# Kernel tuning notes

Measured on AMD Instinct MI355X. Metric: run time of the kernel, lower is better.

## Reference

```python
import jax, jax.numpy as jnp
import numpy as np
import math

N_HEADS = 16
ROPE_THETA = 10000.0


def setup_inputs() -> dict:
    key = jax.random.key(0)
    ks = jax.random.split(key, 5)
    B, S, D = 2, 2048, 2048
    scale = 1.0 / math.sqrt(D)
    hidden_states = jax.random.normal(ks[0], (B, S, D), dtype=jnp.float32)
    attention_mask = jnp.ones((B, S), dtype=jnp.float32)
    Wq = jax.random.normal(ks[1], (D, D), dtype=jnp.float32) * scale
    Wk = jax.random.normal(ks[2], (D, D), dtype=jnp.float32) * scale
    Wv = jax.random.normal(ks[3], (D, D), dtype=jnp.float32) * scale
    Wo = jax.random.normal(ks[4], (D, D), dtype=jnp.float32) * scale
    return {"hidden_states": hidden_states, "attention_mask": attention_mask,
            "Wq": Wq, "Wk": Wk, "Wv": Wv, "Wo": Wo}


def _rope(x, head_dim):
    # x: [B, H, S, hd]
    S = x.shape[2]
    inv_freq = 1.0 / (ROPE_THETA ** (jnp.arange(0, head_dim, 2, dtype=jnp.float32) / head_dim))
    t = jnp.arange(S, dtype=jnp.float32)
    freqs = t[:, None] * inv_freq[None, :]              # [S, hd/2]
    emb = jnp.concatenate([freqs, freqs], axis=-1)      # [S, hd]
    cos = jnp.cos(emb)[None, None, :, :]
    sin = jnp.sin(emb)[None, None, :, :]
    half = head_dim // 2
    x_rot = jnp.concatenate([-x[..., half:], x[..., :half]], axis=-1)
    return x * cos + x_rot * sin


def reference(hidden_states, attention_mask, Wq, Wk, Wv, Wo):
    B, S, D = hidden_states.shape
    H = N_HEADS
    hd = D // H
    # projections (torch Linear: y = x @ W.T), split heads -> [B, H, S, hd]
    q = (hidden_states @ Wq.T).reshape(B, S, H, hd).transpose(0, 2, 1, 3)
    k = (hidden_states @ Wk.T).reshape(B, S, H, hd).transpose(0, 2, 1, 3)
    v = (hidden_states @ Wv.T).reshape(B, S, H, hd).transpose(0, 2, 1, 3)
    q = _rope(q, hd)
    k = _rope(k, hd)
    scores = jnp.einsum('bhqd,bhkd->bhqk', q, k) / jnp.sqrt(jnp.float32(hd))
    causal = jnp.triu(jnp.ones((S, S), dtype=bool), 1)
    scores = jnp.where(causal[None, None, :, :], -jnp.inf, scores)
    # faithful to the source: mask==0 -> -inf, else the mask value is ADDED
    am = attention_mask[:, None, None, :]
    am = jnp.where(am == 0, -jnp.inf, am)
    scores = scores + am
    attn = jax.nn.softmax(scores.astype(jnp.float32), axis=-1).astype(scores.dtype)
    out = jnp.einsum('bhqk,bhkd->bhqd', attn, v)
    out = out.transpose(0, 2, 1, 3).reshape(B, S, D)
    return out @ Wo.T
```

## Files before the change

kernel.cpp:

```cpp
#include <hip/hip_runtime.h>
#include <hip/hip_bf16.h>

typedef unsigned short u16;
using short8 = __attribute__((ext_vector_type(8))) short;
using s16x4  = __attribute__((ext_vector_type(4))) short;
using f32x4  = __attribute__((ext_vector_type(4))) float;

#define S_LEN   2048
#define D_MODEL 2048
#define N_HEADS 16
#define HEAD_DIM 128

__device__ __forceinline__ float bf2f(u16 u) {
  union { unsigned int i; float f; } c; c.i = ((unsigned int)u) << 16; return c.f;
}
__device__ __forceinline__ u16 f2bf(float f) {
  __hip_bfloat16 h = __float2bfloat16(f);
  return *reinterpret_cast<u16*>(&h);
}
__device__ __forceinline__ void gload16(const u16* g, u16* l) {
  __builtin_amdgcn_global_load_lds(
      (const __attribute__((address_space(1))) void*)g,
      (__attribute__((address_space(3))) void*)l, 16, 0, 0);
}
__device__ __forceinline__ unsigned ldsaddr(const void* p) {
  return (unsigned)(size_t)(__attribute__((address_space(3))) const void*)p;
}
template<int CTRL>
__device__ __forceinline__ float dppmov(float v) {
  int i = __builtin_bit_cast(int, v);
  i = __builtin_amdgcn_update_dpp(i, i, CTRL, 0xf, 0xf, false);
  return __builtin_bit_cast(float, i);
}
__device__ __forceinline__ float rowmax16(float x) {
  x = fmaxf(x, dppmov<0x121>(x));
  x = fmaxf(x, dppmov<0x122>(x));
  x = fmaxf(x, dppmov<0x124>(x));
  x = fmaxf(x, dppmov<0x128>(x));
  return x;
}
__device__ __forceinline__ float rowsum16(float x) {
  x += dppmov<0x121>(x);
  x += dppmov<0x122>(x);
  x += dppmov<0x124>(x);
  x += dppmov<0x128>(x);
  return x;
}

__global__ void f2bf_kernel(const float* __restrict__ in, u16* __restrict__ out, int n4) {
  int id = blockIdx.x * 256 + threadIdx.x;
  if (id < n4) {
    float4 v = ((const float4*)in)[id];
    ushort4 o;
    o.x = f2bf(v.x); o.y = f2bf(v.y); o.z = f2bf(v.z); o.w = f2bf(v.w);
    ((ushort4*)out)[id] = o;
  }
}

__global__ void rope_table(float* __restrict__ ct, float* __restrict__ st) {
  int id = blockIdx.x * 256 + threadIdx.x;
  int s = id >> 6, dd = id & 63;
  float inv = powf(10000.0f, -(float)dd * (1.0f / 64.0f));
  float fr = (float)s * inv;
  ct[id] = cosf(fr);
  st[id] = sinf(fr);
}

__global__ __launch_bounds__(256, 2)
void gemm_qkv(const u16* __restrict__ A, const u16* __restrict__ B,
              u16* __restrict__ QKV,
              const float* __restrict__ ct, const float* __restrict__ st) {
  __shared__ u16 As[128 * 64];
  __shared__ u16 Bs[128 * 64];
  const int K = D_MODEL;
  const int tid = threadIdx.x;
  const int lane = tid & 63;
  const int wave = tid >> 6;
  const int wr = wave >> 1, wc = wave & 1;
  const int lo = lane & 15, hi = lane >> 4;
  const int bn = blockIdx.x, bm = blockIdx.y;

  f32x4 acc[4][4];
  const f32x4 z4 = {0.f, 0.f, 0.f, 0.f};
#pragma unroll
  for (int i = 0; i < 4; ++i)
#pragma unroll
    for (int j = 0; j < 4; ++j) acc[i][j] = z4;

  const u16* Abase = A + (size_t)(bm * 128) * K;
  const u16* Bbase = B + (size_t)(bn * 128) * K;

  for (int kt = 0; kt < K; kt += 64) {
#pragma unroll
    for (int i = 0; i < 4; ++i) {
      int p = tid + i * 256;
      int row = p >> 3, cp = p & 7;
      int c = cp ^ (row & 7);
      gload16(Abase + (size_t)row * K + kt + c * 8, &As[p * 8]);
      gload16(Bbase + (size_t)row * K + kt + c * 8, &Bs[p * 8]);
    }
    __syncthreads();
#pragma unroll
    for (int ks = 0; ks < 2; ++ks) {
      short8 af[4], bf[4];
#pragma unroll
      for (int mi = 0; mi < 4; ++mi) {
        int row = wr * 64 + mi * 16 + lo;
        int phys = (ks * 4 + hi) ^ (row & 7);
        af[mi] = *(const short8*)&As[row * 64 + phys * 8];
      }
#pragma unroll
      for (int ni = 0; ni < 4; ++ni) {
        int row = wc * 16 + (ni & 1) * 32 + (ni >> 1) * 64 + lo;
        int phys = (ks * 4 + hi) ^ (row & 7);
        bf[ni] = *(const short8*)&Bs[row * 64 + phys * 8];
      }
#pragma unroll
      for (int mi = 0; mi < 4; ++mi)
#pragma unroll
        for (int ni = 0; ni < 4; ++ni)
          acc[mi][ni] = __builtin_amdgcn_mfma_f32_16x16x32_bf16(af[mi], bf[ni], acc[mi][ni], 0, 0, 0);
    }
    __syncthreads();
  }

  const int r0 = bm * 128 + wr * 64;
  const int tensor = bn >> 4;
  u16* out = QKV + (size_t)tensor * ((size_t)2 * S_LEN * D_MODEL) + (bn & 15) * 128;
  if (tensor < 2) {
#pragma unroll
    for (int mi = 0; mi < 4; ++mi)
#pragma unroll
      for (int j = 0; j < 4; ++j) {
        int row = r0 + mi * 16 + hi * 4 + j;
        int s = row & (S_LEN - 1);
#pragma unroll
        for (int p = 0; p < 2; ++p) {
          int dd = wc * 16 + p * 32 + lo;
          float c = ct[s * 64 + dd], sn = st[s * 64 + dd];
          float x1 = acc[mi][p][j], x2 = acc[mi][p + 2][j];
          out[(size_t)row * D_MODEL + dd]      = f2bf(x1 * c - x2 * sn);
          out[(size_t)row * D_MODEL + dd + 64] = f2bf(x2 * c + x1 * sn);
        }
      }
  } else {
#pragma unroll
    for (int mi = 0; mi < 4; ++mi)
#pragma unroll
      for (int ni = 0; ni < 4; ++ni) {
        int col = wc * 16 + (ni & 1) * 32 + (ni >> 1) * 64 + lo;
#pragma unroll
        for (int j = 0; j < 4; ++j)
          out[(size_t)(r0 + mi * 16 + hi * 4 + j) * D_MODEL + col] = f2bf(acc[mi][ni][j]);
      }
  }
}

__global__ __launch_bounds__(256, 2)
void gemm_nt_f32(const u16* __restrict__ A, const u16* __restrict__ B,
                 float* __restrict__ C, int M, int N, int K) {
  __shared__ u16 As[128 * 64];
  __shared__ u16 Bs[128 * 64];
  const int tid = threadIdx.x;
  const int lane = tid & 63;
  const int wave = tid >> 6;
  const int wr = wave >> 1, wc = wave & 1;
  const int lo = lane & 15, hi = lane >> 4;
  const int bn = blockIdx.x, bm = blockIdx.y;

  f32x4 acc[4][4];
  const f32x4 z4 = {0.f, 0.f, 0.f, 0.f};
#pragma unroll
  for (int i = 0; i < 4; ++i)
#pragma unroll
    for (int j = 0; j < 4; ++j) acc[i][j] = z4;

  const u16* Abase = A + (size_t)(bm * 128) * K;
  const u16* Bbase = B + (size_t)(bn * 128) * K;

  for (int kt = 0; kt < K; kt += 64) {
#pragma unroll
    for (int i = 0; i < 4; ++i) {
      int p = tid + i * 256;
      int row = p >> 3, cp = p & 7;
      int c = cp ^ (row & 7);
      gload16(Abase + (size_t)row * K + kt + c * 8, &As[p * 8]);
      gload16(Bbase + (size_t)row * K + kt + c * 8, &Bs[p * 8]);
    }
    __syncthreads();
#pragma unroll
    for (int ks = 0; ks < 2; ++ks) {
      short8 af[4], bf[4];
#pragma unroll
      for (int mi = 0; mi < 4; ++mi) {
        int row = wr * 64 + mi * 16 + lo;
        int phys = (ks * 4 + hi) ^ (row & 7);
        af[mi] = *(const short8*)&As[row * 64 + phys * 8];
      }
#pragma unroll
      for (int ni = 0; ni < 4; ++ni) {
        int row = wc * 64 + ni * 16 + lo;
        int phys = (ks * 4 + hi) ^ (row & 7);
        bf[ni] = *(const short8*)&Bs[row * 64 + phys * 8];
      }
#pragma unroll
      for (int mi = 0; mi < 4; ++mi)
#pragma unroll
        for (int ni = 0; ni < 4; ++ni)
          acc[mi][ni] = __builtin_amdgcn_mfma_f32_16x16x32_bf16(af[mi], bf[ni], acc[mi][ni], 0, 0, 0);
    }
    __syncthreads();
  }

  const int r0 = bm * 128 + wr * 64;
  const int c0 = bn * 128 + wc * 64;
#pragma unroll
  for (int mi = 0; mi < 4; ++mi)
#pragma unroll
    for (int ni = 0; ni < 4; ++ni)
#pragma unroll
      for (int j = 0; j < 4; ++j)
        C[(size_t)(r0 + mi * 16 + hi * 4 + j) * N + c0 + ni * 16 + lo] = acc[mi][ni][j];
}

__device__ __forceinline__ void stage_tiles(const u16* __restrict__ Kb,
                                            const u16* __restrict__ Vb,
                                            int b, int h, int k0,
                                            u16* ksd, u16* vsd, int tid) {
#pragma unroll
  for (int i = 0; i < 4; ++i) {
    int p = tid + i * 256;
    int r = p >> 4, cp = p & 15;
    int c = cp ^ (r & 15);
    gload16(Kb + ((size_t)(b * S_LEN + k0 + r) * D_MODEL + h * HEAD_DIM + c * 8), ksd + p * 8);
  }
#pragma unroll
  for (int i = 0; i < 4; ++i) {
    int p = tid + i * 256;
    int k = ((p >> 6) << 2) | ((p >> 1) & 3);
    int d = (((p >> 3) & 7) << 4) | ((p & 1) << 3);
    gload16(Vb + ((size_t)(b * S_LEN + k0 + k) * D_MODEL + h * HEAD_DIM + d), vsd + p * 8);
  }
}

__global__ __launch_bounds__(256, 2)
void attn_fwd(const u16* __restrict__ Qb, const u16* __restrict__ Kb,
              const u16* __restrict__ Vb, u16* __restrict__ AOb) {
  __shared__ u16 Ks[2][64 * 128];
  __shared__ u16 Vs[2][64 * 128];
  __shared__ u16 Ps[4][16 * 70];

  const int tid = threadIdx.x, lane = tid & 63, wave = tid >> 6;
  const int lo = lane & 15, hi = lane >> 4;
  const int wgid = blockIdx.x;
  const int xcd = wgid & 7;
  const int qidx = (wgid >> 3) & 31;
  const int bh = ((wgid >> 8) << 3) | xcd;
  const int qb = 31 - qidx;
  const int b = bh >> 4, h = bh & 15;
  const float scale = 0.08838834764831845f;
  const f32x4 z4 = {0.f, 0.f, 0.f, 0.f};

  const int q0 = qb * 64;
  const int wq0 = q0 + wave * 16;

  short8 qa[4];
  {
    const u16* qbase = Qb + ((size_t)(b * S_LEN + wq0) * D_MODEL + h * HEAD_DIM);
#pragma unroll
    for (int ks = 0; ks < 4; ++ks)
      qa[ks] = *(const short8*)(qbase + (size_t)lo * D_MODEL + ks * 32 + hi * 8);
  }

  f32x4 oacc[8];
  float mrow[4], lrow[4];
#pragma unroll
  for (int nf = 0; nf < 8; ++nf) oacc[nf] = z4;
#pragma unroll
  for (int j = 0; j < 4; ++j) { mrow[j] = -1e30f; lrow[j] = 0.f; }

  u16* pw = Ps[wave];
  const int nkv = qb + 1;

  stage_tiles(Kb, Vb, b, h, 0, &Ks[0][0], &Vs[0][0], tid);
  asm volatile("s_waitcnt vmcnt(0)" ::: "memory");
  __builtin_amdgcn_s_barrier();
  __builtin_amdgcn_sched_barrier(0);

  int cur = 0;
  for (int kv = 0; kv < nkv; ++kv) {
    const int k0 = kv * 64;
    if (kv + 1 < nkv)
      stage_tiles(Kb, Vb, b, h, k0 + 64, &Ks[cur ^ 1][0], &Vs[cur ^ 1][0], tid);

    const u16* ksb = &Ks[cur][0];
    const unsigned vtr_base = ldsaddr(&Vs[cur][0]) + hi * 2048u + lo * 8u;

    f32x4 sacc[4];
#pragma unroll
    for (int nf = 0; nf < 4; ++nf) sacc[nf] = z4;
    __builtin_amdgcn_s_setprio(1);
#pragma unroll
    for (int ks = 0; ks < 4; ++ks) {
      short8 kb[4];
#pragma unroll
      for (int nf = 0; nf < 4; ++nf) {
        int r = nf * 16 + lo;
        int phys = (ks * 4 + hi) ^ (r & 15);
        kb[nf] = *(const short8*)&ksb[r * 128 + phys * 8];
      }
#pragma unroll
      for (int nf = 0; nf < 4; ++nf)
        sacc[nf] = __builtin_amdgcn_mfma_f32_16x16x32_bf16(qa[ks], kb[nf], sacc[nf], 0, 0, 0);
    }
    __builtin_amdgcn_s_setprio(0);

    float rm[4];
#pragma unroll
    for (int j = 0; j < 4; ++j) {
      const int qrow = wq0 + hi * 4 + j;
      float mx = -1e30f;
#pragma unroll
      for (int nf = 0; nf < 4; ++nf) {
        int kcol = k0 + nf * 16 + lo;
        float v = sacc[nf][j] * scale;
        v = (kcol <= qrow) ? v : -1e30f;
        sacc[nf][j] = v;
        mx = fmaxf(mx, v);
      }
      rm[j] = rowmax16(mx);
    }
    float growth = fmaxf(fmaxf(rm[0] - mrow[0], rm[1] - mrow[1]),
                         fmaxf(rm[2] - mrow[2], rm[3] - mrow[3]));
    if (!__all(growth <= 8.0f)) {
#pragma unroll
      for (int j = 0; j < 4; ++j) {
        float mn = fmaxf(mrow[j], rm[j]);
        float alpha = __expf(mrow[j] - mn);
        mrow[j] = mn;
        lrow[j] *= alpha;
#pragma unroll
        for (int nf = 0; nf < 8; ++nf) oacc[nf][j] *= alpha;
      }
    }
#pragma unroll
    for (int j = 0; j < 4; ++j) {
      float rs = 0.f;
#pragma unroll
      for (int nf = 0; nf < 4; ++nf) {
        float p = __expf(sacc[nf][j] - mrow[j]);
        sacc[nf][j] = p;
        rs += p;
      }
      lrow[j] += rowsum16(rs);
    }
#pragma unroll
    for (int nf = 0; nf < 4; ++nf)
#pragma unroll
      for (int j = 0; j < 4; ++j)
        pw[(hi * 4 + j) * 70 + nf * 16 + lo] = f2bf(sacc[nf][j]);
#pragma unroll
    for (int ks2 = 0; ks2 < 2; ++ks2) {
      short8 pa = *(const short8*)&pw[lo * 70 + ks2 * 32 + hi * 8];
      s16x4 t0[8], t1[8];
#pragma unroll
      for (int r = 0; r < 8; ++r) {
        unsigned a = vtr_base + ks2 * 8192u + r * 128u;
        asm volatile("ds_read_b64_tr_b16 %0, %1" : "=v"(t0[r]) : "v"(a));
        asm volatile("ds_read_b64_tr_b16 %0, %1" : "=v"(t1[r]) : "v"(a + 1024u));
      }
      asm volatile("s_waitcnt lgkmcnt(0)" ::: "memory");
      __builtin_amdgcn_sched_barrier(0);
      __builtin_amdgcn_s_setprio(1);
#pragma unroll
      for (int r = 0; r < 8; ++r) {
        short8 vb = __builtin_shufflevector(t0[r], t1[r], 0, 1, 2, 3, 4, 5, 6, 7);
        oacc[r] = __builtin_amdgcn_mfma_f32_16x16x32_bf16(pa, vb, oacc[r], 0, 0, 0);
      }
      __builtin_amdgcn_s_setprio(0);
    }

    asm volatile("s_waitcnt vmcnt(0)" ::: "memory");
    __builtin_amdgcn_s_barrier();
    __builtin_amdgcn_sched_barrier(0);
    cur ^= 1;
  }

  float inv[4];
#pragma unroll
  for (int j = 0; j < 4; ++j) inv[j] = 1.0f / lrow[j];
  u16* obase = AOb + ((size_t)(b * S_LEN + wq0) * D_MODEL + h * HEAD_DIM);
#pragma unroll
  for (int nf = 0; nf < 8; ++nf)
#pragma unroll
    for (int j = 0; j < 4; ++j)
      obase[(size_t)(hi * 4 + j) * D_MODEL + nf * 16 + lo] = f2bf(oacc[nf][j] * inv[j]);
}

extern "C" void kernel_launch(void* const* d_in, const int* in_sizes, int n_in,
                              void* d_out, int out_size, void* d_ws, size_t ws_size,
                              hipStream_t stream) {
  const float* hs = (const float*)d_in[0];
  const float* Wq = (const float*)d_in[2];
  const float* Wk = (const float*)d_in[3];
  const float* Wv = (const float*)d_in[4];
  const float* Wo = (const float*)d_in[5];

  const size_t HS_B = (size_t)4096 * 2048 * 2;
  const size_t W_B  = (size_t)2048 * 2048 * 2;
  const size_t T_B  = (size_t)2048 * 64 * 4;

  char* w = (char*)d_ws;
  u16* HSb = (u16*)w;            w += HS_B;
  u16* Wqb = (u16*)w;            w += W_B;
  u16* Wkb = (u16*)w;            w += W_B;
  u16* Wvb = (u16*)w;            w += W_B;
  u16* Wob = (u16*)w;            w += W_B;
  u16* Qb  = (u16*)w;            w += HS_B;
  u16* Kb  = (u16*)w;            w += HS_B;
  u16* Vb  = (u16*)w;            w += HS_B;
  float* ct = (float*)w;         w += T_B;
  float* st = (float*)w;         w += T_B;
  if (ws_size < (size_t)(w - (char*)d_ws)) return;

  u16* AOb = HSb;

  f2bf_kernel<<<2097152 / 256, 256, 0, stream>>>(hs, HSb, 2097152);
  f2bf_kernel<<<1048576 / 256, 256, 0, stream>>>(Wq, Wqb, 1048576);
  f2bf_kernel<<<1048576 / 256, 256, 0, stream>>>(Wk, Wkb, 1048576);
  f2bf_kernel<<<1048576 / 256, 256, 0, stream>>>(Wv, Wvb, 1048576);
  f2bf_kernel<<<1048576 / 256, 256, 0, stream>>>(Wo, Wob, 1048576);
  rope_table<<<(2048 * 64) / 256, 256, 0, stream>>>(ct, st);

  gemm_qkv<<<dim3(48, 32), 256, 0, stream>>>(HSb, Wqb, Qb, ct, st);

  attn_fwd<<<dim3(1024), 256, 0, stream>>>(Qb, Kb, Vb, AOb);

  gemm_nt_f32<<<dim3(16, 32), 256, 0, stream>>>(AOb, Wob, (float*)d_out, 4096, 2048, 2048);
}
```

Baseline: 276.5 us.

## Pair causal q-blocks per workgroup, fold softmax scale into Q, fuse weight casts

```diff
diff --git a/kernel.cpp b/kernel.cpp
--- a/kernel.cpp
+++ b/kernel.cpp
@@ -55,6 +55,17 @@
     o.x = f2bf(v.x); o.y = f2bf(v.y); o.z = f2bf(v.z); o.w = f2bf(v.w);
     ((ushort4*)out)[id] = o;
   }
+}
+__global__ void f2bf4_kernel(const float* __restrict__ w0, const float* __restrict__ w1,
+                             const float* __restrict__ w2, const float* __restrict__ w3,
+                             u16* __restrict__ out) {
+  const int n4 = 1048576;
+  const float* in = (blockIdx.y == 0) ? w0 : (blockIdx.y == 1) ? w1 : (blockIdx.y == 2) ? w2 : w3;
+  int id = blockIdx.x * 256 + threadIdx.x;
+  float4 v = ((const float4*)in)[id];
+  ushort4 o;
+  o.x = f2bf(v.x); o.y = f2bf(v.y); o.z = f2bf(v.z); o.w = f2bf(v.w);
+  ((ushort4*)(out + (size_t)blockIdx.y * n4 * 4))[id] = o;
 }
 
 __global__ void rope_table(float* __restrict__ ct, float* __restrict__ st) {
@@ -128,6 +139,7 @@
   const int tensor = bn >> 4;
   u16* out = QKV + (size_t)tensor * ((size_t)2 * S_LEN * D_MODEL) + (bn & 15) * 128;
   if (tensor < 2) {
+    const float qs = (tensor == 0) ? 0.08838834764831845f : 1.0f;
 #pragma unroll
     for (int mi = 0; mi < 4; ++mi)
 #pragma unroll
@@ -137,7 +149,7 @@
 #pragma unroll
         for (int p = 0; p < 2; ++p) {
           int dd = wc * 16 + p * 32 + lo;
-          float c = ct[s * 64 + dd], sn = st[s * 64 + dd];
+          float c = ct[s * 64 + dd] * qs, sn = st[s * 64 + dd] * qs;
           float x1 = acc[mi][p][j], x2 = acc[mi][p + 2][j];
           out[(size_t)row * D_MODEL + dd]      = f2bf(x1 * c - x2 * sn);
           out[(size_t)row * D_MODEL + dd + 64] = f2bf(x2 * c + x1 * sn);
@@ -253,148 +265,157 @@
   const int tid = threadIdx.x, lane = tid & 63, wave = tid >> 6;
   const int lo = lane & 15, hi = lane >> 4;
   const int wgid = blockIdx.x;
-  const int xcd = wgid & 7;
-  const int qidx = (wgid >> 3) & 31;
-  const int bh = ((wgid >> 8) << 3) | xcd;
-  const int qb = 31 - qidx;
+  const int idx = (wgid >> 3) & 15;
+  const int bh = ((wgid >> 7) << 3) | (wgid & 7);
   const int b = bh >> 4, h = bh & 15;
-  const float scale = 0.08838834764831845f;
   const f32x4 z4 = {0.f, 0.f, 0.f, 0.f};
-
-  const int q0 = qb * 64;
-  const int wq0 = q0 + wave * 16;
-
-  short8 qa[4];
-  {
-    const u16* qbase = Qb + ((size_t)(b * S_LEN + wq0) * D_MODEL + h * HEAD_DIM);
-#pragma unroll
-    for (int ks = 0; ks < 4; ++ks)
-      qa[ks] = *(const short8*)(qbase + (size_t)lo * D_MODEL + ks * 32 + hi * 8);
-  }
-
-  f32x4 oacc[8];
-  float mrow[4], lrow[4];
-#pragma unroll
-  for (int nf = 0; nf < 8; ++nf) oacc[nf] = z4;
-#pragma unroll
-  for (int j = 0; j < 4; ++j) { mrow[j] = -1e30f; lrow[j] = 0.f; }
-
   u16* pw = Ps[wave];
-  const int nkv = qb + 1;
-
-  stage_tiles(Kb, Vb, b, h, 0, &Ks[0][0], &Vs[0][0], tid);
-  asm volatile("s_waitcnt vmcnt(0)" ::: "memory");
-  __builtin_amdgcn_s_barrier();
-  __builtin_amdgcn_sched_barrier(0);
-
-  int cur = 0;
-  for (int kv = 0; kv < nkv; ++kv) {
-    const int k0 = kv * 64;
-    if (kv + 1 < nkv)
-      stage_tiles(Kb, Vb, b, h, k0 + 64, &Ks[cur ^ 1][0], &Vs[cur ^ 1][0], tid);
-
-    const u16* ksb = &Ks[cur][0];
-    const unsigned vtr_base = ldsaddr(&Vs[cur][0]) + hi * 2048u + lo * 8u;
-
-    f32x4 sacc[4];
-#pragma unroll
-    for (int nf = 0; nf < 4; ++nf) sacc[nf] = z4;
-    __builtin_amdgcn_s_setprio(1);
-#pragma unroll
-    for (int ks = 0; ks < 4; ++ks) {
-      short8 kb[4];
-#pragma unroll
-      for (int nf = 0; nf < 4; ++nf) {
-        int r = nf * 16 + lo;
-        int phys = (ks * 4 + hi) ^ (r & 15);
-        kb[nf] = *(const short8*)&ksb[r * 128 + phys * 8];
-      }
-#pragma unroll
-      for (int nf = 0; nf < 4; ++nf)
-        sacc[nf] = __builtin_amdgcn_mfma_f32_16x16x32_bf16(qa[ks], kb[nf], sacc[nf], 0, 0, 0);
-    }
-    __builtin_amdgcn_s_setprio(0);
-
-    float rm[4];
-#pragma unroll
-    for (int j = 0; j < 4; ++j) {
-      const int qrow = wq0 + hi * 4 + j;
-      float mx = -1e30f;
-#pragma unroll
-      for (int nf = 0; nf < 4; ++nf) {
-        int kcol = k0 + nf * 16 + lo;
-        float v = sacc[nf][j] * scale;
-        v = (kcol <= qrow) ? v : -1e30f;
-        sacc[nf][j] = v;
-        mx = fmaxf(mx, v);
-      }
-      rm[j] = rowmax16(mx);
-    }
-    float growth = fmaxf(fmaxf(rm[0] - mrow[0], rm[1] - mrow[1]),
-                         fmaxf(rm[2] - mrow[2], rm[3] - mrow[3]));
-    if (!__all(growth <= 8.0f)) {
-#pragma unroll
-      for (int j = 0; j < 4; ++j) {
-        float mn = fmaxf(mrow[j], rm[j]);
-        float alpha = __expf(mrow[j] - mn);
-        mrow[j] = mn;
-        lrow[j] *= alpha;
-#pragma unroll
-        for (int nf = 0; nf < 8; ++nf) oacc[nf][j] *= alpha;
-      }
-    }
-#pragma unroll
-    for (int j = 0; j < 4; ++j) {
-      float rs = 0.f;
-#pragma unroll
-      for (int nf = 0; nf < 4; ++nf) {
-        float p = __expf(sacc[nf][j] - mrow[j]);
-        sacc[nf][j] = p;
-        rs += p;
-      }
-      lrow[j] += rowsum16(rs);
-    }
-#pragma unroll
-    for (int nf = 0; nf < 4; ++nf)
-#pragma unroll
-      for (int j = 0; j < 4; ++j)
-        pw[(hi * 4 + j) * 70 + nf * 16 + lo] = f2bf(sacc[nf][j]);
-#pragma unroll
-    for (int ks2 = 0; ks2 < 2; ++ks2) {
-      short8 pa = *(const short8*)&pw[lo * 70 + ks2 * 32 + hi * 8];
-      s16x4 t0[8], t1[8];
-#pragma unroll
-      for (int r = 0; r < 8; ++r) {
-        unsigned a = vtr_base + ks2 * 8192u + r * 128u;
-        asm volatile("ds_read_b64_tr_b16 %0, %1" : "=v"(t0[r]) : "v"(a));
-        asm volatile("ds_read_b64_tr_b16 %0, %1" : "=v"(t1[r]) : "v"(a + 1024u));
-      }
-      asm volatile("s_waitcnt lgkmcnt(0)" ::: "memory");
-      __builtin_amdgcn_sched_barrier(0);
-      __builtin_amdgcn_s_setprio(1);
-#pragma unroll
-      for (int r = 0; r < 8; ++r) {
-        short8 vb = __builtin_shufflevector(t0[r], t1[r], 0, 1, 2, 3, 4, 5, 6, 7);
-        oacc[r] = __builtin_amdgcn_mfma_f32_16x16x32_bf16(pa, vb, oacc[r], 0, 0, 0);
-      }
-      __builtin_amdgcn_s_setprio(0);
-    }
-
+
+  for (int pass = 0; pass < 2; ++pass) {
+    const int qb = pass ? (31 - idx) : idx;
+    const int wq0 = qb * 64 + wave * 16;
+
+    short8 qa[4];
+    {
+      const u16* qbase = Qb + ((size_t)(b * S_LEN + wq0) * D_MODEL + h * HEAD_DIM);
+#pragma unroll
+      for (int ks = 0; ks < 4; ++ks)
+        qa[ks] = *(const short8*)(qbase + (size_t)lo * D_MODEL + ks * 32 + hi * 8);
+    }
+
+    f32x4 oacc[8];
+    float mrow[4], lrow[4];
+#pragma unroll
+    for (int nf = 0; nf < 8; ++nf) oacc[nf] = z4;
+#pragma unroll
+    for (int j = 0; j < 4; ++j) { mrow[j] = -1e30f; lrow[j] = 0.f; }
+
+    const int nkv = qb + 1;
+
+    stage_tiles(Kb, Vb, b, h, 0, &Ks[0][0], &Vs[0][0], tid);
     asm volatile("s_waitcnt vmcnt(0)" ::: "memory");
     __builtin_amdgcn_s_barrier();
     __builtin_amdgcn_sched_barrier(0);
-    cur ^= 1;
-  }
-
-  float inv[4];
-#pragma unroll
-  for (int j = 0; j < 4; ++j) inv[j] = 1.0f / lrow[j];
-  u16* obase = AOb + ((size_t)(b * S_LEN + wq0) * D_MODEL + h * HEAD_DIM);
-#pragma unroll
-  for (int nf = 0; nf < 8; ++nf)
-#pragma unroll
-    for (int j = 0; j < 4; ++j)
-      obase[(size_t)(hi * 4 + j) * D_MODEL + nf * 16 + lo] = f2bf(oacc[nf][j] * inv[j]);
+
+    int cur = 0;
+    for (int kv = 0; kv < nkv; ++kv) {
+      const int k0 = kv * 64;
+      if (kv + 1 < nkv)
+        stage_tiles(Kb, Vb, b, h, k0 + 64, &Ks[cur ^ 1][0], &Vs[cur ^ 1][0], tid);
+
+      if (k0 <= wq0 + 15) {
+        const u16* ksb = &Ks[cur][0];
+        const unsigned vtr_base = ldsaddr(&Vs[cur][0]) + hi * 2048u + lo * 8u;
+
+        f32x4 sacc[4];
+#pragma unroll
+        for (int nf = 0; nf < 4; ++nf) sacc[nf] = z4;
+        __builtin_amdgcn_s_setprio(1);
+#pragma unroll
+        for (int ks = 0; ks < 4; ++ks) {
+          short8 kb[4];
+#pragma unroll
+          for (int nf = 0; nf < 4; ++nf) {
+            int r = nf * 16 + lo;
+            int phys = (ks * 4 + hi) ^ (r & 15);
+            kb[nf] = *(const short8*)&ksb[r * 128 + phys * 8];
+          }
+#pragma unroll
+          for (int nf = 0; nf < 4; ++nf)
+            sacc[nf] = __builtin_amdgcn_mfma_f32_16x16x32_bf16(qa[ks], kb[nf], sacc[nf], 0, 0, 0);
+        }
+        __builtin_amdgcn_s_setprio(0);
+
+        float rm[4];
+        if (k0 + 63 > wq0) {
+#pragma unroll
+          for (int j = 0; j < 4; ++j) {
+            const int qrow = wq0 + hi * 4 + j;
+            float mx = -1e30f;
+#pragma unroll
+            for (int nf = 0; nf < 4; ++nf) {
+              int kcol = k0 + nf * 16 + lo;
+              float v = sacc[nf][j];
+              v = (kcol <= qrow) ? v : -1e30f;
+              sacc[nf][j] = v;
+              mx = fmaxf(mx, v);
+            }
+            rm[j] = rowmax16(mx);
+          }
+        } else {
+#pragma unroll
+          for (int j = 0; j < 4; ++j) {
+            float mx = fmaxf(fmaxf(sacc[0][j], sacc[1][j]), fmaxf(sacc[2][j], sacc[3][j]));
+            rm[j] = rowmax16(mx);
+          }
+        }
+        float growth = fmaxf(fmaxf(rm[0] - mrow[0], rm[1] - mrow[1]),
+                             fmaxf(rm[2] - mrow[2], rm[3] - mrow[3]));
+        if (!__all(growth <= 8.0f)) {
+#pragma unroll
+          for (int j = 0; j < 4; ++j) {
+            float mn = fmaxf(mrow[j], rm[j]);
+            float alpha = __expf(mrow[j] - mn);
+            mrow[j] = mn;
+            lrow[j] *= alpha;
+#pragma unroll
+            for (int nf = 0; nf < 8; ++nf) oacc[nf][j] *= alpha;
+          }
+        }
+#pragma unroll
+        for (int j = 0; j < 4; ++j) {
+          float rs = 0.f;
+#pragma unroll
+          for (int nf = 0; nf < 4; ++nf) {
+            float p = __expf(sacc[nf][j] - mrow[j]);
+            sacc[nf][j] = p;
+            rs += p;
+          }
+          lrow[j] += rowsum16(rs);
+        }
+#pragma unroll
+        for (int nf = 0; nf < 4; ++nf)
+#pragma unroll
+          for (int j = 0; j < 4; ++j)
+            pw[(hi * 4 + j) * 70 + nf * 16 + lo] = f2bf(sacc[nf][j]);
+#pragma unroll
+        for (int ks2 = 0; ks2 < 2; ++ks2) {
+          short8 pa = *(const short8*)&pw[lo * 70 + ks2 * 32 + hi * 8];
+          s16x4 t0[8], t1[8];
+#pragma unroll
+          for (int r = 0; r < 8; ++r) {
+            unsigned a = vtr_base + ks2 * 8192u + r * 128u;
+            asm volatile("ds_read_b64_tr_b16 %0, %1" : "=v"(t0[r]) : "v"(a));
+            asm volatile("ds_read_b64_tr_b16 %0, %1" : "=v"(t1[r]) : "v"(a + 1024u));
+          }
+          asm volatile("s_waitcnt lgkmcnt(0)" ::: "memory");
+          __builtin_amdgcn_sched_barrier(0);
+          __builtin_amdgcn_s_setprio(1);
+#pragma unroll
+          for (int r = 0; r < 8; ++r) {
+            short8 vb = __builtin_shufflevector(t0[r], t1[r], 0, 1, 2, 3, 4, 5, 6, 7);
+            oacc[r] = __builtin_amdgcn_mfma_f32_16x16x32_bf16(pa, vb, oacc[r], 0, 0, 0);
+          }
+          __builtin_amdgcn_s_setprio(0);
+        }
+      }
+
+      asm volatile("s_waitcnt vmcnt(0)" ::: "memory");
+      __builtin_amdgcn_s_barrier();
+      __builtin_amdgcn_sched_barrier(0);
+      cur ^= 1;
+    }
+
+    float inv[4];
+#pragma unroll
+    for (int j = 0; j < 4; ++j) inv[j] = 1.0f / lrow[j];
+    u16* obase = AOb + ((size_t)(b * S_LEN + wq0) * D_MODEL + h * HEAD_DIM);
+#pragma unroll
+    for (int nf = 0; nf < 8; ++nf)
+#pragma unroll
+      for (int j = 0; j < 4; ++j)
+        obase[(size_t)(hi * 4 + j) * D_MODEL + nf * 16 + lo] = f2bf(oacc[nf][j] * inv[j]);
+  }
 }
 
 extern "C" void kernel_launch(void* const* d_in, const int* in_sizes, int n_in,
@@ -426,15 +447,12 @@
   u16* AOb = HSb;
 
   f2bf_kernel<<<2097152 / 256, 256, 0, stream>>>(hs, HSb, 2097152);
-  f2bf_kernel<<<1048576 / 256, 256, 0, stream>>>(Wq, Wqb, 1048576);
-  f2bf_kernel<<<1048576 / 256, 256, 0, stream>>>(Wk, Wkb, 1048576);
-  f2bf_kernel<<<1048576 / 256, 256, 0, stream>>>(Wv, Wvb, 1048576);
-  f2bf_kernel<<<1048576 / 256, 256, 0, stream>>>(Wo, Wob, 1048576);
+  f2bf4_kernel<<<dim3(1048576 / 256, 4), 256, 0, stream>>>(Wq, Wk, Wv, Wo, Wqb);
   rope_table<<<(2048 * 64) / 256, 256, 0, stream>>>(ct, st);
 
   gemm_qkv<<<dim3(48, 32), 256, 0, stream>>>(HSb, Wqb, Qb, ct, st);
 
-  attn_fwd<<<dim3(1024), 256, 0, stream>>>(Qb, Kb, Vb, AOb);
+  attn_fwd<<<dim3(512), 256, 0, stream>>>(Qb, Kb, Vb, AOb);
 
   gemm_nt_f32<<<dim3(16, 32), 256, 0, stream>>>(AOb, Wob, (float*)d_out, 4096, 2048, 2048);
 }
```

Result: faster. 237.4 us (-14.1%).
